# Kernel optimization log

Hardware: AMD Instinct MI355X
Metric: run time of the kernel (lower is better)

## Reference

```python
import jax, jax.numpy as jnp
import numpy as np

NUM_CLASSES = 19
IGNORE_INDEX = 255
FOCAL_GAMMA = 3.0
FOCAL_WEIGHT = 1.0
EPS = 1e-6


def setup_inputs() -> dict:
    key = jax.random.key(0)
    k1, k2 = jax.random.split(key)
    logits = jax.random.normal(k1, (8, NUM_CLASSES, 512, 512), dtype=jnp.float32)
    targets = jax.random.randint(k2, (8, 512, 512), 0, NUM_CLASSES, dtype=jnp.int64)
    return {"logits": logits, "targets": targets}


def reference(logits, targets):
    C = NUM_CLASSES
    # [B,C,H,W] -> [N,C] log-probs, N = B*H*W
    logp = jax.nn.log_softmax(logits, axis=1)
    lp = jnp.transpose(logp, (0, 2, 3, 1)).reshape(-1, C)
    t = targets.reshape(-1)
    valid = (t != IGNORE_INDEX)
    tc = jnp.clip(t, 0, C - 1)  # safe index for ignored pixels
    validf = valid.astype(lp.dtype)
    n_valid = jnp.maximum(jnp.sum(validf), 1.0)

    # mean cross entropy over valid pixels (F.cross_entropy with ignore_index)
    nll = -jnp.take_along_axis(lp, tc[:, None], axis=1)[:, 0]
    ce = jnp.sum(nll * validf) / n_valid

    # per-class focal term: -log(p_t) * (1 - p_t)^gamma, p_t clamped to [1e-6, 1]
    pt = jnp.clip(jnp.exp(-nll), EPS, 1.0)
    focal_terms = -jnp.log(pt) * (1.0 - pt) ** FOCAL_GAMMA

    # single-pass segment reduce: per-class sum and count over valid pixels
    sums = jax.ops.segment_sum(focal_terms * validf, tc, num_segments=C)
    counts = jax.ops.segment_sum(validf, tc, num_segments=C)
    present = counts > 0
    per_class_mean = sums / jnp.maximum(counts, 1.0)
    n_present = jnp.maximum(jnp.sum(present.astype(lp.dtype)), 1.0)
    focal = jnp.sum(jnp.where(present, per_class_mean, 0.0)) / n_present

    return ce + FOCAL_WEIGHT * focal
```

## Files before the change

kernel.cpp:

```cpp
#include <hip/hip_runtime.h>


#define NCLS 19
#define IGNORE_IDX 255
#define HW4 65536
#define FOCAL_EPS 1e-6f
#define NBLK 2048
#define NQ 40

__global__ __launch_bounds__(256, 8) void focal_main(
        const float* __restrict__ logits,
        const int*   __restrict__ targets,
        float* __restrict__ P) {
    __shared__ float    s_csum[NCLS];
    __shared__ unsigned s_ccnt[NCLS];
    __shared__ float    s_wnll[4];
    __shared__ int      s_wcnt[4];

    const int tid = threadIdx.x;
    if (tid < NCLS) { s_csum[tid] = 0.0f; s_ccnt[tid] = 0u; }
    __syncthreads();

    const unsigned g = blockIdx.x * 256u + tid;
    const unsigned b = g >> 16;
    const unsigned q = g & 65535u;
    const float4* base = reinterpret_cast<const float4*>(logits)
                         + (size_t)b * (NCLS * (size_t)HW4) + q;

    const int4 t4 = reinterpret_cast<const int4*>(targets)[g];
    int tt[4] = { t4.x, t4.y, t4.z, t4.w };
    int tc[4];
    bool fval[4];
#pragma unroll
    for (int j = 0; j < 4; ++j) {
        tc[j]   = min(max(tt[j], 0), NCLS - 1);
        fval[j] = (tt[j] != IGNORE_IDX);
    }

    float s[4]  = {0.0f, 0.0f, 0.0f, 0.0f};
    float xt[4] = {0.0f, 0.0f, 0.0f, 0.0f};
#pragma unroll
    for (int c = 0; c < NCLS; ++c) {
        const float4 v = base[(size_t)c * HW4];
        const float vv[4] = { v.x, v.y, v.z, v.w };
#pragma unroll
        for (int j = 0; j < 4; ++j) {
            s[j] += __expf(vv[j]);
            if (c == tc[j]) xt[j] = vv[j];
        }
    }

    float nll_acc = 0.0f;
    int   vcnt    = 0;
#pragma unroll
    for (int j = 0; j < 4; ++j) {
        const float lse = __logf(s[j]);
        const float nll = lse - xt[j];

        float pt = __expf(-nll);
        pt = fminf(fmaxf(pt, FOCAL_EPS), 1.0f);
        const float om = 1.0f - pt;
        const float f  = -__logf(pt) * om * om * om;

        if (fval[j]) {
            nll_acc += nll; ++vcnt;
            atomicAdd(&s_csum[tc[j]], f);
            atomicAdd(&s_ccnt[tc[j]], 1u);
        }
    }

#pragma unroll
    for (int off = 32; off > 0; off >>= 1) {
        nll_acc += __shfl_down(nll_acc, off);
        vcnt    += __shfl_down(vcnt, off);
    }
    const int wid = tid >> 6, lane = tid & 63;
    if (lane == 0) { s_wnll[wid] = nll_acc; s_wcnt[wid] = vcnt; }
    __syncthreads();

    const unsigned bid = blockIdx.x;
    if (tid == 0) {
        float bn = s_wnll[0] + s_wnll[1] + s_wnll[2] + s_wnll[3];
        int   bc = s_wcnt[0] + s_wcnt[1] + s_wcnt[2] + s_wcnt[3];
        P[0 * NBLK + bid] = bn;
        P[1 * NBLK + bid] = (float)bc;
    }
    if (tid < NCLS) {
        P[(2 + tid) * NBLK + bid]        = s_csum[tid];
        P[(2 + NCLS + tid) * NBLK + bid] = (float)s_ccnt[tid];
    }
}

__global__ __launch_bounds__(1024) void focal_final(
        const float* __restrict__ P, float* __restrict__ out) {
    __shared__ double s_q[NQ];
    const int tid  = threadIdx.x;
    const int wid  = tid >> 6;
    const int lane = tid & 63;

    for (int q = wid; q < NQ; q += 16) {
        double v = 0.0;
#pragma unroll
        for (int k = 0; k < NBLK / 64; ++k)
            v += (double)P[q * NBLK + lane + 64 * k];
#pragma unroll
        for (int off = 32; off > 0; off >>= 1)
            v += __shfl_down(v, off);
        if (lane == 0) s_q[q] = v;
    }
    __syncthreads();

    if (tid == 0) {
        double nv = s_q[1];
        if (nv < 1.0) nv = 1.0;
        const double ce = s_q[0] / nv;

        double fsum = 0.0, npres = 0.0;
        for (int c = 0; c < NCLS; ++c) {
            const double cnt = s_q[2 + NCLS + c];
            if (cnt > 0.0) {
                fsum += s_q[2 + c] / (cnt < 1.0 ? 1.0 : cnt);
                npres += 1.0;
            }
        }
        if (npres < 1.0) npres = 1.0;
        out[0] = (float)(ce + fsum / npres);
    }
}

extern "C" void kernel_launch(void* const* d_in, const int* in_sizes, int n_in,
                              void* d_out, int out_size, void* d_ws, size_t ws_size,
                              hipStream_t stream) {
    const float* logits  = (const float*)d_in[0];
    const int*   targets = (const int*)d_in[1];
    float*       out     = (float*)d_out;
    float*       P       = (float*)d_ws;

    focal_main<<<NBLK, 256, 0, stream>>>(logits, targets, P);
    focal_final<<<1, 1024, 0, stream>>>(P, out);
}
```

Baseline: 277.5 us.

## Stage logits tiles into LDS via async global_load_lds before per-pixel compute

Each block now processes two 512-pixel tiles. For each tile it copies all 19 class planes into shared memory using the async global-to-LDS load builtin, then each thread reads one pixel at a time from LDS instead of doing four-pixel float4 register loads. This is meant to improve memory-level parallelism and coalescing of the strided class loads. In exchange it uses about 38 KB of LDS per block, which lowers occupancy, and it adds barriers between the load and compute phases with no overlap of the two.

```diff
diff --git a/kernel.cpp b/kernel.cpp
--- a/kernel.cpp
+++ b/kernel.cpp
@@ -7,11 +7,15 @@
 #define FOCAL_EPS 1e-6f
 #define NBLK 2048
 #define NQ 40
+#define TILE4 128
+#define TPIX 512
+#define SLOTS (NCLS*TILE4)
 
-__global__ __launch_bounds__(256, 8) void focal_main(
+__global__ __launch_bounds__(256) void focal_main(
         const float* __restrict__ logits,
         const int*   __restrict__ targets,
         float* __restrict__ P) {
+    __shared__ float    lds[NCLS * TPIX];
     __shared__ float    s_csum[NCLS];
     __shared__ unsigned s_ccnt[NCLS];
     __shared__ float    s_wnll[4];
@@ -19,54 +23,63 @@
 
     const int tid = threadIdx.x;
     if (tid < NCLS) { s_csum[tid] = 0.0f; s_ccnt[tid] = 0u; }
-    __syncthreads();
-
-    const unsigned g = blockIdx.x * 256u + tid;
-    const unsigned b = g >> 16;
-    const unsigned q = g & 65535u;
-    const float4* base = reinterpret_cast<const float4*>(logits)
-                         + (size_t)b * (NCLS * (size_t)HW4) + q;
-
-    const int4 t4 = reinterpret_cast<const int4*>(targets)[g];
-    int tt[4] = { t4.x, t4.y, t4.z, t4.w };
-    int tc[4];
-    bool fval[4];
-#pragma unroll
-    for (int j = 0; j < 4; ++j) {
-        tc[j]   = min(max(tt[j], 0), NCLS - 1);
-        fval[j] = (tt[j] != IGNORE_IDX);
-    }
-
-    float s[4]  = {0.0f, 0.0f, 0.0f, 0.0f};
-    float xt[4] = {0.0f, 0.0f, 0.0f, 0.0f};
-#pragma unroll
-    for (int c = 0; c < NCLS; ++c) {
-        const float4 v = base[(size_t)c * HW4];
-        const float vv[4] = { v.x, v.y, v.z, v.w };
-#pragma unroll
-        for (int j = 0; j < 4; ++j) {
-            s[j] += __expf(vv[j]);
-            if (c == tc[j]) xt[j] = vv[j];
-        }
-    }
 
     float nll_acc = 0.0f;
     int   vcnt    = 0;
+
+    for (int tt = 0; tt < 2; ++tt) {
+        const int tile = blockIdx.x * 2 + tt;
+        const int b    = tile >> 9;
+        const int tq   = (tile & 511) * TILE4;
+        const float4* ibase = reinterpret_cast<const float4*>(logits)
+                              + (size_t)b * (NCLS * (size_t)HW4) + tq;
+
 #pragma unroll
-    for (int j = 0; j < 4; ++j) {
-        const float lse = __logf(s[j]);
-        const float nll = lse - xt[j];
+        for (int it = 0; it < 10; ++it) {
+            const int slot = it * 256 + tid;
+            if (slot < SLOTS) {
+                const int c   = slot >> 7;
+                const int off = slot & 127;
+                const float4* src = ibase + (size_t)c * HW4 + off;
+                __builtin_amdgcn_global_load_lds(
+                    (const __attribute__((address_space(1))) unsigned*)src,
+                    (__attribute__((address_space(3))) unsigned*)
+                        ((char*)lds + (size_t)slot * 16),
+                    16, 0, 0);
+            }
+        }
+        __syncthreads();
 
-        float pt = __expf(-nll);
-        pt = fminf(fmaxf(pt, FOCAL_EPS), 1.0f);
-        const float om = 1.0f - pt;
-        const float f  = -__logf(pt) * om * om * om;
+        const int pixbase = tile * TPIX;
+#pragma unroll
+        for (int h = 0; h < 2; ++h) {
+            const int pix = tid + h * 256;
+            const int t   = targets[pixbase + pix];
+            const int tc  = min(max(t, 0), NCLS - 1);
+            const bool valid = (t != IGNORE_IDX);
 
-        if (fval[j]) {
-            nll_acc += nll; ++vcnt;
-            atomicAdd(&s_csum[tc[j]], f);
-            atomicAdd(&s_ccnt[tc[j]], 1u);
+            float s = 0.0f, xt = 0.0f;
+#pragma unroll
+            for (int c = 0; c < NCLS; ++c) {
+                const float v = lds[c * TPIX + pix];
+                s += __expf(v);
+                if (c == tc) xt = v;
+            }
+            const float lse = __logf(s);
+            const float nll = lse - xt;
+
+            float pt = __expf(-nll);
+            pt = fminf(fmaxf(pt, FOCAL_EPS), 1.0f);
+            const float om = 1.0f - pt;
+            const float f  = -__logf(pt) * om * om * om;
+
+            if (valid) {
+                nll_acc += nll; ++vcnt;
+                atomicAdd(&s_csum[tc], f);
+                atomicAdd(&s_ccnt[tc], 1u);
+            }
         }
+        __syncthreads();
     }
 
 #pragma unroll
```

Result: faster. 235.7 us (-15.1%).
